# Kernel optimization log

Hardware: AMD Instinct MI355X
Metric: run time of the kernel (lower is better)

Reference implementation:

```python
import jax, jax.numpy as jnp
import numpy as np

EPS = 1e-8  # EPSILON in original repo (sharpen denom); cosine eps matches torch default 1e-8
MAX_SHIFT = 1
M_FEAT = 128


def _lstm_cell(x, h, c, W_ih, W_hh, b_ih, b_hh):
    gates = x @ W_ih.T + b_ih + h @ W_hh.T + b_hh
    i, f, g, o = jnp.split(gates, 4, axis=1)
    c_new = jax.nn.sigmoid(f) * c + jax.nn.sigmoid(i) * jnp.tanh(g)
    h_new = jax.nn.sigmoid(o) * jnp.tanh(c_new)
    return h_new, c_new


def _content_address(bank, k, b):
    # torch cosine_similarity over dim 2: dot / max(|m||k|, eps)
    dot = jnp.einsum('bnm,bm->bn', bank, k)
    denom = jnp.maximum(jnp.linalg.norm(bank, axis=2) * jnp.linalg.norm(k, axis=1, keepdims=True), 1e-8)
    return jax.nn.softmax(b * dot / denom, axis=1)


def _shift(w, s):
    # circular unroll then valid cross-correlation with per-batch kernel s [B, 2*MAX_SHIFT+1]
    wp = jnp.concatenate([w[:, -MAX_SHIFT:], w, w[:, :MAX_SHIFT]], axis=1)
    N = w.shape[1]
    taps = 2 * MAX_SHIFT + 1
    return sum(s[:, i:i + 1] * wp[:, i:i + N] for i in range(taps))


def _sharpen(w, r):
    wr = w ** r
    return wr / (wr.sum(axis=1, keepdims=True) + EPS)


def _move(bank, w_prev, k, b, g, s, r):
    w = _content_address(bank, k, b)
    w = w + (1.0 - g) * w_prev  # faithful: w_c is NOT scaled by g in the source
    w = _shift(w, s)
    return _sharpen(w, r)


def _split_read(p):
    M = M_FEAT
    k = p[:, :M]
    b = jax.nn.softplus(p[:, M:M + 1])
    g = jax.nn.sigmoid(p[:, M + 1:M + 2])
    s = jax.nn.softmax(p[:, M + 2:M + 5], axis=1)
    r = 1.0 + jax.nn.softplus(p[:, M + 5:M + 6])
    return k, b, g, s, r


def _split_write(p):
    M = M_FEAT
    k, b, g, s, r = _split_read(p[:, :M + 6])
    e = jax.nn.sigmoid(p[:, M + 6:M + 6 + M])
    a = p[:, M + 6 + M:M + 6 + 2 * M]
    return k, b, g, s, r, e, a


def setup_inputs() -> dict:
    key = jax.random.key(0)
    ks = jax.random.split(key, 16)
    B, E, H, N, M, O = 64, 256, 512, 4096, 128, 256
    rd_out, wr_out = M + 2 * MAX_SHIFT + 4, 3 * M + 2 * MAX_SHIFT + 4
    sc = 0.05
    return {
        'x': jax.random.normal(ks[0], (B, E), jnp.float32),
        'h_prev': jax.random.normal(ks[1], (B, H), jnp.float32),
        'c_prev': jax.random.normal(ks[2], (B, H), jnp.float32),
        'bank': jax.random.normal(ks[3], (B, N, M), jnp.float32) * 0.1,
        'read_w_prev': jnp.zeros((3, B, N), jnp.float32),
        'write_w_prev': jnp.zeros((3, B, N), jnp.float32),
        'W_ih': jax.random.normal(ks[4], (4 * H, E), jnp.float32) * sc,
        'W_hh': jax.random.normal(ks[5], (4 * H, H), jnp.float32) * sc,
        'b_ih': jax.random.normal(ks[6], (4 * H,), jnp.float32) * sc,
        'b_hh': jax.random.normal(ks[7], (4 * H,), jnp.float32) * sc,
        'read_W': jax.random.normal(ks[8], (3, rd_out, H), jnp.float32) * sc,
        'read_b': jax.random.normal(ks[9], (3, rd_out), jnp.float32) * sc,
        'write_W': jax.random.normal(ks[10], (3, wr_out, H), jnp.float32) * sc,
        'write_b': jax.random.normal(ks[11], (3, wr_out), jnp.float32) * sc,
        'out_W': jax.random.normal(ks[12], (O, 3 * M + H), jnp.float32) * sc,
        'out_b': jax.random.normal(ks[13], (O,), jnp.float32) * sc,
    }


def reference(x, h_prev, c_prev, bank, read_w_prev, write_w_prev,
              W_ih, W_hh, b_ih, b_hh, read_W, read_b, write_W, write_b,
              out_W, out_b):
    h, c = _lstm_cell(x, h_prev, c_prev, W_ih, W_hh, b_ih, b_hh)
    reads = []
    for i in range(3):  # head_num=3, structurally distinct params per head
        # write head: update bank
        pw = h @ write_W[i].T + write_b[i]
        k, b, g, s, r, e, a = _split_write(pw)
        ww = _move(bank, write_w_prev[i], k, b, g, s, r)
        bank = bank * (1.0 - ww[:, :, None] * e[:, None, :]) + ww[:, :, None] * a[:, None, :]
        # read head: read from updated bank
        pr = h @ read_W[i].T + read_b[i]
        k, b, g, s, r = _split_read(pr)
        wr = _move(bank, read_w_prev[i], k, b, g, s, r)
        reads.append(jnp.einsum('bn,bnm->bm', wr, bank))
    out = jnp.concatenate(reads + [h], axis=1) @ out_W.T + out_b
    return out
```

## Files before the change

### kernel.cpp

```cpp
#include <hip/hip_runtime.h>
#include <math.h>

namespace {

constexpr int kB = 64;
constexpr int kN = 4096;
constexpr int kM = 128;
constexpr int kH = 512;
constexpr int kE = 256;
constexpr int kO = 256;
constexpr int kGates = 4 * kH;
constexpr int kCatW = 3 * kM + kH;
constexpr int kPRow = 1600;
constexpr int kWN = kB * kN;

__device__ __forceinline__ float sigm_(float x) { return 1.f / (1.f + expf(-x)); }
__device__ __forceinline__ float softplus_(float x) { return x > 20.f ? x : log1pf(expf(x)); }

__global__ __launch_bounds__(256) void gates_gemm(const float* __restrict__ x,
                                                  const float* __restrict__ W_ih,
                                                  const float* __restrict__ h_prev,
                                                  const float* __restrict__ W_hh,
                                                  float* __restrict__ gates,
                                                  const float* __restrict__ out_b,
                                                  float* __restrict__ out,
                                                  float* __restrict__ cat) {
  if (blockIdx.x == 32) {
    const int tid = threadIdx.x;
    for (int i = tid; i < kB * kO; i += 256) out[i] = out_b[i & (kO - 1)];
    for (int i = tid; i < kB * 384; i += 256) cat[(i / 384) * kCatW + (i % 384)] = 0.f;
    return;
  }
  __shared__ float As[64][68];
  __shared__ float Ws[64][68];
  const int tid = threadIdx.x;
  const int j0 = blockIdx.x * 64;
  const int b0 = (tid & 15) * 4;
  const int j4 = (tid >> 4) * 4;
  float acc[4][4] = {};
  for (int kc = 0; kc < 12; kc++) {
    const bool isx = kc < 4;
    const float* A = isx ? x : h_prev;
    const float* W = isx ? W_ih : W_hh;
    const int lda = isx ? kE : kH;
    const int k0 = (isx ? kc : (kc - 4)) * 64;
    __syncthreads();
#pragma unroll
    for (int i = 0; i < 4; i++) {
      int idx = tid + i * 256;
      int bb = idx >> 4;
      int kk = (idx & 15) * 4;
      float4 v = *(const float4*)(A + (size_t)bb * lda + k0 + kk);
      As[kk][bb] = v.x; As[kk + 1][bb] = v.y; As[kk + 2][bb] = v.z; As[kk + 3][bb] = v.w;
      float4 w = *(const float4*)(W + (size_t)(j0 + bb) * lda + k0 + kk);
      Ws[kk][bb] = w.x; Ws[kk + 1][bb] = w.y; Ws[kk + 2][bb] = w.z; Ws[kk + 3][bb] = w.w;
    }
    __syncthreads();
#pragma unroll 2
    for (int k = 0; k < 64; k++) {
      float4 av = *(const float4*)&As[k][b0];
      float4 wv = *(const float4*)&Ws[k][j4];
      float aa[4] = {av.x, av.y, av.z, av.w};
      float ww[4] = {wv.x, wv.y, wv.z, wv.w};
#pragma unroll
      for (int ii = 0; ii < 4; ii++)
#pragma unroll
        for (int jj = 0; jj < 4; jj++) acc[ii][jj] += aa[ii] * ww[jj];
    }
  }
#pragma unroll
  for (int ii = 0; ii < 4; ii++) {
    float4 st = make_float4(acc[ii][0], acc[ii][1], acc[ii][2], acc[ii][3]);
    *(float4*)&gates[(size_t)(b0 + ii) * kGates + j0 + j4] = st;
  }
}

__global__ __launch_bounds__(256) void lstm_nl(const float* __restrict__ gates,
                                               const float* __restrict__ b_ih,
                                               const float* __restrict__ b_hh,
                                               const float* __restrict__ c_prev,
                                               float* __restrict__ cat) {
  int idx = blockIdx.x * 256 + threadIdx.x;
  if (idx >= kB * kH) return;
  int b = idx >> 9;
  int hh = idx & (kH - 1);
  const float* g = gates + (size_t)b * kGates;
  float i_ = g[hh]          + b_ih[hh]          + b_hh[hh];
  float f_ = g[kH + hh]     + b_ih[kH + hh]     + b_hh[kH + hh];
  float g_ = g[2 * kH + hh] + b_ih[2 * kH + hh] + b_hh[2 * kH + hh];
  float o_ = g[3 * kH + hh] + b_ih[3 * kH + hh] + b_hh[3 * kH + hh];
  float c = sigm_(f_) * c_prev[idx] + sigm_(i_) * tanhf(g_);
  cat[(size_t)b * kCatW + 3 * kM + hh] = sigm_(o_) * tanhf(c);
}

__global__ __launch_bounds__(256) void proj_gemm(const float* __restrict__ cat,
                                                 const float* __restrict__ write_W,
                                                 const float* __restrict__ read_W,
                                                 float* __restrict__ praw) {
  __shared__ float As[64][68];
  __shared__ float Ws[64][68];
  const float* A = cat + 3 * kM;
  const int tid = threadIdx.x;
  const int j0 = blockIdx.x * 64;
  const int b0 = (tid & 15) * 4;
  const int j4 = (tid >> 4) * 4;
  float acc[4][4] = {};
  for (int kc = 0; kc < 8; kc++) {
    const int k0 = kc * 64;
    __syncthreads();
#pragma unroll
    for (int i = 0; i < 4; i++) {
      int idx = tid + i * 256;
      int bb = idx >> 4;
      int kk = (idx & 15) * 4;
      float4 v = *(const float4*)(A + (size_t)bb * kCatW + k0 + kk);
      As[kk][bb] = v.x; As[kk + 1][bb] = v.y; As[kk + 2][bb] = v.z; As[kk + 3][bb] = v.w;
      int j = j0 + bb;
      float4 w = make_float4(0.f, 0.f, 0.f, 0.f);
      if (j < 1170)      w = *(const float4*)(write_W + (size_t)j * kH + k0 + kk);
      else if (j < 1572) w = *(const float4*)(read_W + (size_t)(j - 1170) * kH + k0 + kk);
      Ws[kk][bb] = w.x; Ws[kk + 1][bb] = w.y; Ws[kk + 2][bb] = w.z; Ws[kk + 3][bb] = w.w;
    }
    __syncthreads();
#pragma unroll 2
    for (int k = 0; k < 64; k++) {
      float4 av = *(const float4*)&As[k][b0];
      float4 wv = *(const float4*)&Ws[k][j4];
      float aa[4] = {av.x, av.y, av.z, av.w};
      float ww[4] = {wv.x, wv.y, wv.z, wv.w};
#pragma unroll
      for (int ii = 0; ii < 4; ii++)
#pragma unroll
        for (int jj = 0; jj < 4; jj++) acc[ii][jj] += aa[ii] * ww[jj];
    }
  }
  if (j0 + j4 < 1572) {
#pragma unroll
    for (int ii = 0; ii < 4; ii++) {
      float4 st = make_float4(acc[ii][0], acc[ii][1], acc[ii][2], acc[ii][3]);
      *(float4*)&praw[(size_t)(b0 + ii) * kPRow + j0 + j4] = st;
    }
  }
}

__global__ __launch_bounds__(128) void split_params(const float* __restrict__ praw,
                                                    const float* __restrict__ write_b,
                                                    const float* __restrict__ read_b,
                                                    float* __restrict__ kwb, float* __restrict__ krb,
                                                    float* __restrict__ evb, float* __restrict__ avb,
                                                    float* __restrict__ scal,
                                                    float* __restrict__ sdot) {
  const int b = blockIdx.x;
  const int m = threadIdx.x;
  __shared__ float red[2];
  for (int i = 0; i < 3; i++) {
    const float* p = praw + (size_t)b * kPRow + i * 390;
    const float* wb = write_b + i * 390;
    float kv = p[m] + wb[m];
    kwb[((size_t)i * kB + b) * kM + m] = kv;
    evb[((size_t)i * kB + b) * kM + m] = sigm_(p[134 + m] + wb[134 + m]);
    avb[((size_t)i * kB + b) * kM + m] = p[262 + m] + wb[262 + m];
    float sq = kv * kv;
#pragma unroll
    for (int mm = 1; mm < 64; mm <<= 1) sq += __shfl_xor(sq, mm, 64);
    __syncthreads();
    if ((m & 63) == 0) red[m >> 6] = sq;
    __syncthreads();
    if (m == 0) {
      float* s = scal + ((size_t)i * kB + b) * 8;
      s[0] = softplus_(p[128] + wb[128]);
      s[1] = sigm_(p[129] + wb[129]);
      s[2] = 1.f + softplus_(p[133] + wb[133]);
      float x0 = p[130] + wb[130], x1 = p[131] + wb[131], x2 = p[132] + wb[132];
      float mx = fmaxf(x0, fmaxf(x1, x2));
      float e0 = expf(x0 - mx), e1 = expf(x1 - mx), e2 = expf(x2 - mx);
      float si = 1.f / (e0 + e1 + e2);
      s[3] = e0 * si; s[4] = e1 * si; s[5] = e2 * si;
      s[6] = sqrtf(red[0] + red[1]);
    }
    __syncthreads();
  }
  for (int i = 0; i < 3; i++) {
    const float* p = praw + (size_t)b * kPRow + 1170 + i * 134;
    const float* rb = read_b + i * 134;
    float kv = p[m] + rb[m];
    krb[((size_t)i * kB + b) * kM + m] = kv;
    float sq = kv * kv;
#pragma unroll
    for (int mm = 1; mm < 64; mm <<= 1) sq += __shfl_xor(sq, mm, 64);
    __syncthreads();
    if ((m & 63) == 0) red[m >> 6] = sq;
    __syncthreads();
    if (m == 0) {
      float* s = scal + ((size_t)(3 + i) * kB + b) * 8;
      s[0] = softplus_(p[128] + rb[128]);
      s[1] = sigm_(p[129] + rb[129]);
      s[2] = 1.f + softplus_(p[133] + rb[133]);
      float x0 = p[130] + rb[130], x1 = p[131] + rb[131], x2 = p[132] + rb[132];
      float mx = fmaxf(x0, fmaxf(x1, x2));
      float e0 = expf(x0 - mx), e1 = expf(x1 - mx), e2 = expf(x2 - mx);
      float si = 1.f / (e0 + e1 + e2);
      s[3] = e0 * si; s[4] = e1 * si; s[5] = e2 * si;
      s[6] = sqrtf(red[0] + red[1]);
    }
    __syncthreads();
  }
  __syncthreads();
  if (m < 64) {
    const float* a0 = avb + ((size_t)0 * kB + b) * kM;
    const float* a2 = avb + ((size_t)2 * kB + b) * kM;
    const float* u[5] = {a0, a0, a0, a2, a2};
    const float* v[5] = {krb + ((size_t)0 * kB + b) * kM,
                         kwb + ((size_t)1 * kB + b) * kM,
                         a0,
                         krb + ((size_t)2 * kB + b) * kM,
                         a2};
#pragma unroll
    for (int d = 0; d < 5; d++) {
      float s = u[d][m] * v[d][m] + u[d][m + 64] * v[d][m + 64];
#pragma unroll
      for (int mm = 1; mm < 64; mm <<= 1) s += __shfl_xor(s, mm, 64);
      if (m == 0) sdot[b * 8 + d] = s;
    }
  }
}

__global__ __launch_bounds__(256) void passA_k(const float* __restrict__ bank,
                                               const float* __restrict__ kwb,
                                               const float* __restrict__ krb,
                                               const float* __restrict__ evb,
                                               const float* __restrict__ avb,
                                               float* __restrict__ mA) {
  const int b = blockIdx.y, chunk = blockIdx.x;
  const int tid = threadIdx.x;
  const int lane = tid & 63, wv = tid >> 6, sub = lane >> 4, lm = lane & 15;
  const int m8 = lm * 8;
  float kw0r[8], kr0r[8], kw1r[8], a0r[8], e0r[8];
#pragma unroll
  for (int t = 0; t < 8; t++) {
    kw0r[t] = kwb[((size_t)0 * kB + b) * kM + m8 + t];
    kr0r[t] = krb[((size_t)0 * kB + b) * kM + m8 + t];
    kw1r[t] = kwb[((size_t)1 * kB + b) * kM + m8 + t];
    a0r[t]  = avb[((size_t)0 * kB + b) * kM + m8 + t];
    e0r[t]  = evb[((size_t)0 * kB + b) * kM + m8 + t];
  }
  const size_t bbase = (size_t)b * kN * kM;
  const size_t brow = (size_t)b * kN;
  for (int it = 0; it < 16; it++) {
    const int row = chunk * 256 + it * 16 + wv * 4 + sub;
    const float* rp = bank + bbase + (size_t)row * kM + m8;
    float4 u0 = *(const float4*)rp;
    float4 u1 = *(const float4*)(rp + 4);
    float v[8] = {u0.x, u0.y, u0.z, u0.w, u1.x, u1.y, u1.z, u1.w};
    float s[10] = {};
#pragma unroll
    for (int t = 0; t < 8; t++) {
      float be = v[t] * e0r[t];
      s[0] += v[t] * kw0r[t];
      s[1] += v[t] * v[t];
      s[2] += v[t] * kr0r[t];
      s[3] += be * kr0r[t];
      s[4] += v[t] * kw1r[t];
      s[5] += be * kw1r[t];
      s[6] += be * v[t];
      s[7] += be * be;
      s[8] += v[t] * a0r[t];
      s[9] += be * a0r[t];
    }
#pragma unroll
    for (int m = 1; m < 16; m <<= 1)
#pragma unroll
      for (int k = 0; k < 10; k++) s[k] += __shfl_xor(s[k], m, 64);
    if (lm == 0) {
#pragma unroll
      for (int k = 0; k < 10; k++) mA[(size_t)k * kWN + brow + row] = s[k];
    }
  }
}

__device__ void addr_core(int tid, float* loc, const float* sc, const float* __restrict__ wp,
                          float* wb, float* red) {
  const float g = sc[1], r = sc[2];
  const float s0 = sc[3], s1 = sc[4], s2 = sc[5];
  const int lane = tid & 63, wid = tid >> 6;
  __syncthreads();
  float mx = -1e30f;
#pragma unroll
  for (int i = 0; i < 16; i++) mx = fmaxf(mx, loc[i]);
#pragma unroll
  for (int m = 1; m < 64; m <<= 1) mx = fmaxf(mx, __shfl_xor(mx, m, 64));
  if (lane == 0) red[wid] = mx;
  __syncthreads();
  mx = fmaxf(fmaxf(red[0], red[1]), fmaxf(red[2], red[3]));
  float sum = 0.f;
#pragma unroll
  for (int i = 0; i < 16; i++) { loc[i] = expf(loc[i] - mx); sum += loc[i]; }
#pragma unroll
  for (int m = 1; m < 64; m <<= 1) sum += __shfl_xor(sum, m, 64);
  __syncthreads();
  if (lane == 0) red[wid] = sum;
  __syncthreads();
  sum = red[0] + red[1] + red[2] + red[3];
  const float inv = 1.f / sum;
  const float omg = 1.f - g;
#pragma unroll
  for (int i = 0; i < 16; i++) {
    int n = tid + i * 256;
    wb[n] = loc[i] * inv + omg * wp[n];
  }
  __syncthreads();
  float ssum = 0.f;
#pragma unroll
  for (int i = 0; i < 16; i++) {
    int n = tid + i * 256;
    float sh = s0 * wb[(n + kN - 1) & (kN - 1)] + s1 * wb[n] + s2 * wb[(n + 1) & (kN - 1)];
    float y = powf(sh, r);
    loc[i] = y;
    ssum += y;
  }
#pragma unroll
  for (int m = 1; m < 64; m <<= 1) ssum += __shfl_xor(ssum, m, 64);
  __syncthreads();
  if (lane == 0) red[wid] = ssum;
  __syncthreads();
  ssum = red[0] + red[1] + red[2] + red[3];
  const float invs = 1.f / (ssum + 1e-8f);
#pragma unroll
  for (int i = 0; i < 16; i++) loc[i] *= invs;
}

__global__ __launch_bounds__(256) void a12_k(const float* __restrict__ mA,
                                             const float* __restrict__ scal,
                                             const float* __restrict__ sdot,
                                             const float* __restrict__ read_w_prev,
                                             const float* __restrict__ write_w_prev,
                                             float* __restrict__ wwv,
                                             float* __restrict__ wrv) {
  const int b = blockIdx.x;
  const int tid = threadIdx.x;
  __shared__ float wb[kN];
  __shared__ float red[4];
  const size_t brow = (size_t)b * kN;
  float loc[16], w0r[16], q1r[16];
  {
    const float* sc = scal + ((size_t)0 * kB + b) * 8;
    const float beta = sc[0], kn = sc[6];
#pragma unroll
    for (int i = 0; i < 16; i++) {
      size_t idx = brow + tid + i * 256;
      float d = mA[0 * (size_t)kWN + idx];
      float q = mA[1 * (size_t)kWN + idx];
      loc[i] = beta * d / fmaxf(sqrtf(fmaxf(q, 0.f)) * kn, 1e-8f);
    }
    addr_core(tid, loc, sc, write_w_prev + brow, wb, red);
#pragma unroll
    for (int i = 0; i < 16; i++) { wwv[brow + tid + i * 256] = loc[i]; w0r[i] = loc[i]; }
  }
  {
    const float* sc = scal + ((size_t)3 * kB + b) * 8;
    const float beta = sc[0], kn = sc[6];
    const float sa0kr0 = sdot[b * 8 + 0], sa0a0 = sdot[b * 8 + 2];
#pragma unroll
    for (int i = 0; i < 16; i++) {
      size_t idx = brow + tid + i * 256;
      float w0 = w0r[i], w0q = w0 * w0;
      float q1 = mA[1 * (size_t)kWN + idx]
               - 2.f * w0 * mA[6 * (size_t)kWN + idx]
               + w0q * mA[7 * (size_t)kWN + idx]
               + 2.f * w0 * mA[8 * (size_t)kWN + idx]
               - 2.f * w0q * mA[9 * (size_t)kWN + idx]
               + w0q * sa0a0;
      q1r[i] = q1;
      float d = mA[2 * (size_t)kWN + idx] - w0 * mA[3 * (size_t)kWN + idx] + w0 * sa0kr0;
      loc[i] = beta * d / fmaxf(sqrtf(fmaxf(q1, 0.f)) * kn, 1e-8f);
    }
    addr_core(tid, loc, sc, read_w_prev + brow, wb, red);
#pragma unroll
    for (int i = 0; i < 16; i++) wrv[brow + tid + i * 256] = loc[i];
  }
  {
    const float* sc = scal + ((size_t)1 * kB + b) * 8;
    const float beta = sc[0], kn = sc[6];
    const float sa0kw1 = sdot[b * 8 + 1];
#pragma unroll
    for (int i = 0; i < 16; i++) {
      size_t idx = brow + tid + i * 256;
      float w0 = w0r[i];
      float d = mA[4 * (size_t)kWN + idx] - w0 * mA[5 * (size_t)kWN + idx] + w0 * sa0kw1;
      loc[i] = beta * d / fmaxf(sqrtf(fmaxf(q1r[i], 0.f)) * kn, 1e-8f);
    }
    addr_core(tid, loc, sc, write_w_prev + kWN + brow, wb, red);
#pragma unroll
    for (int i = 0; i < 16; i++) wwv[kWN + brow + tid + i * 256] = loc[i];
  }
}

__global__ __launch_bounds__(256) void passB_k(const float* __restrict__ bank,
                                               const float* __restrict__ wwv,
                                               const float* __restrict__ wrv,
                                               const float* __restrict__ kwb,
                                               const float* __restrict__ krb,
                                               const float* __restrict__ evb,
                                               const float* __restrict__ avb,
                                               float* __restrict__ cat,
                                               float* __restrict__ mB) {
  const int b = blockIdx.y, chunk = blockIdx.x;
  const int tid = threadIdx.x;
  const int lane = tid & 63, wv = tid >> 6, sub = lane >> 4, lm = lane & 15;
  const int m8 = lm * 8;
  float e0r[8], a0r[8], e1r[8], a1r[8], kr1r[8], kw2r[8], kr2r[8], e2r[8], a2r[8];
#pragma unroll
  for (int t = 0; t < 8; t++) {
    e0r[t]  = evb[((size_t)0 * kB + b) * kM + m8 + t];
    a0r[t]  = avb[((size_t)0 * kB + b) * kM + m8 + t];
    e1r[t]  = evb[((size_t)1 * kB + b) * kM + m8 + t];
    a1r[t]  = avb[((size_t)1 * kB + b) * kM + m8 + t];
    kr1r[t] = krb[((size_t)1 * kB + b) * kM + m8 + t];
    kw2r[t] = kwb[((size_t)2 * kB + b) * kM + m8 + t];
    kr2r[t] = krb[((size_t)2 * kB + b) * kM + m8 + t];
    e2r[t]  = evb[((size_t)2 * kB + b) * kM + m8 + t];
    a2r[t]  = avb[((size_t)2 * kB + b) * kM + m8 + t];
  }
  float racc[8] = {};
  __shared__ float rlds[kM];
  if (tid < kM) rlds[tid] = 0.f;
  const size_t bbase = (size_t)b * kN * kM;
  const size_t brow = (size_t)b * kN;
  for (int it = 0; it < 16; it++) {
    const int row = chunk * 256 + it * 16 + wv * 4 + sub;
    const float* rp = bank + bbase + (size_t)row * kM + m8;
    float4 u0 = *(const float4*)rp;
    float4 u1 = *(const float4*)(rp + 4);
    float v[8] = {u0.x, u0.y, u0.z, u0.w, u1.x, u1.y, u1.z, u1.w};
    const float w0 = wwv[brow + row];
    const float w1 = wwv[kWN + brow + row];
    const float wr0 = wrv[brow + row];
#pragma unroll
    for (int t = 0; t < 8; t++) {
      v[t] += w0 * (a0r[t] - e0r[t] * v[t]);
      racc[t] += wr0 * v[t];
      v[t] += w1 * (a1r[t] - e1r[t] * v[t]);
    }
    float s[9] = {};
#pragma unroll
    for (int t = 0; t < 8; t++) {
      float ve = v[t] * e2r[t];
      s[0] += v[t] * kr1r[t];
      s[1] += v[t] * kw2r[t];
      s[2] += v[t] * v[t];
      s[3] += v[t] * kr2r[t];
      s[4] += ve * kr2r[t];
      s[5] += ve * v[t];
      s[6] += ve * ve;
      s[7] += v[t] * a2r[t];
      s[8] += ve * a2r[t];
    }
#pragma unroll
    for (int m = 1; m < 16; m <<= 1)
#pragma unroll
      for (int k = 0; k < 9; k++) s[k] += __shfl_xor(s[k], m, 64);
    if (lm == 0) {
#pragma unroll
      for (int k = 0; k < 9; k++) mB[(size_t)k * kWN + brow + row] = s[k];
    }
  }
  __syncthreads();
#pragma unroll
  for (int t = 0; t < 8; t++) {
    racc[t] += __shfl_xor(racc[t], 16, 64);
    racc[t] += __shfl_xor(racc[t], 32, 64);
  }
  if (sub == 0) {
#pragma unroll
    for (int t = 0; t < 8; t++) atomicAdd(&rlds[m8 + t], racc[t]);
  }
  __syncthreads();
  if (tid < kM) atomicAdd(&cat[(size_t)b * kCatW + tid], rlds[tid]);
}

__global__ __launch_bounds__(256) void a34_k(const float* __restrict__ mB,
                                             const float* __restrict__ scal,
                                             const float* __restrict__ sdot,
                                             const float* __restrict__ read_w_prev,
                                             const float* __restrict__ write_w_prev,
                                             float* __restrict__ wwv,
                                             float* __restrict__ wrv) {
  const int b = blockIdx.x;
  const int tid = threadIdx.x;
  __shared__ float wb[kN];
  __shared__ float red[4];
  const size_t brow = (size_t)b * kN;
  float loc[16], w2r[16];
  {
    const float* sc = scal + ((size_t)4 * kB + b) * 8;
    const float beta = sc[0], kn = sc[6];
#pragma unroll
    for (int i = 0; i < 16; i++) {
      size_t idx = brow + tid + i * 256;
      float d = mB[0 * (size_t)kWN + idx];
      float q = mB[2 * (size_t)kWN + idx];
      loc[i] = beta * d / fmaxf(sqrtf(fmaxf(q, 0.f)) * kn, 1e-8f);
    }
    addr_core(tid, loc, sc, read_w_prev + kWN + brow, wb, red);
#pragma unroll
    for (int i = 0; i < 16; i++) wrv[kWN + brow + tid + i * 256] = loc[i];
  }
  {
    const float* sc = scal + ((size_t)2 * kB + b) * 8;
    const float beta = sc[0], kn = sc[6];
#pragma unroll
    for (int i = 0; i < 16; i++) {
      size_t idx = brow + tid + i * 256;
      float d = mB[1 * (size_t)kWN + idx];
      float q = mB[2 * (size_t)kWN + idx];
      loc[i] = beta * d / fmaxf(sqrtf(fmaxf(q, 0.f)) * kn, 1e-8f);
    }
    addr_core(tid, loc, sc, write_w_prev + 2 * kWN + brow, wb, red);
#pragma unroll
    for (int i = 0; i < 16; i++) { wwv[2 * (size_t)kWN + brow + tid + i * 256] = loc[i]; w2r[i] = loc[i]; }
  }
  {
    const float* sc = scal + ((size_t)5 * kB + b) * 8;
    const float beta = sc[0], kn = sc[6];
    const float sa2kr2 = sdot[b * 8 + 3], sa2a2 = sdot[b * 8 + 4];
#pragma unroll
    for (int i = 0; i < 16; i++) {
      size_t idx = brow + tid + i * 256;
      float w2 = w2r[i], w2q = w2 * w2;
      float q3 = mB[2 * (size_t)kWN + idx]
               - 2.f * w2 * mB[5 * (size_t)kWN + idx]
               + w2q * mB[6 * (size_t)kWN + idx]
               + 2.f * w2 * mB[7 * (size_t)kWN + idx]
               - 2.f * w2q * mB[8 * (size_t)kWN + idx]
               + w2q * sa2a2;
      float d = mB[3 * (size_t)kWN + idx] - w2 * mB[4 * (size_t)kWN + idx] + w2 * sa2kr2;
      loc[i] = beta * d / fmaxf(sqrtf(fmaxf(q3, 0.f)) * kn, 1e-8f);
    }
    addr_core(tid, loc, sc, read_w_prev + 2 * kWN + brow, wb, red);
#pragma unroll
    for (int i = 0; i < 16; i++) wrv[2 * (size_t)kWN + brow + tid + i * 256] = loc[i];
  }
}

__global__ __launch_bounds__(256) void passC_k(const float* __restrict__ bank,
                                               const float* __restrict__ wwv,
                                               const float* __restrict__ wrv,
                                               const float* __restrict__ evb,
                                               const float* __restrict__ avb,
                                               float* __restrict__ cat) {
  const int b = blockIdx.y, chunk = blockIdx.x;
  const int tid = threadIdx.x;
  const int lane = tid & 63, wv = tid >> 6, sub = lane >> 4, lm = lane & 15;
  const int m8 = lm * 8;
  float e_r[3][8], a_r[3][8];
#pragma unroll
  for (int j = 0; j < 3; j++)
#pragma unroll
    for (int t = 0; t < 8; t++) {
      e_r[j][t] = evb[((size_t)j * kB + b) * kM + m8 + t];
      a_r[j][t] = avb[((size_t)j * kB + b) * kM + m8 + t];
    }
  float racc1[8] = {}, racc2[8] = {};
  __shared__ float rlds[2][kM];
  if (tid < kM) { rlds[0][tid] = 0.f; rlds[1][tid] = 0.f; }
  const size_t bbase = (size_t)b * kN * kM;
  const size_t brow = (size_t)b * kN;
  for (int it = 0; it < 16; it++) {
    const int row = chunk * 256 + it * 16 + wv * 4 + sub;
    const float* rp = bank + bbase + (size_t)row * kM + m8;
    float4 u0 = *(const float4*)rp;
    float4 u1 = *(const float4*)(rp + 4);
    float v[8] = {u0.x, u0.y, u0.z, u0.w, u1.x, u1.y, u1.z, u1.w};
    const float w0 = wwv[brow + row];
    const float w1 = wwv[kWN + brow + row];
    const float w2 = wwv[2 * (size_t)kWN + brow + row];
    const float wr1 = wrv[kWN + brow + row];
    const float wr2 = wrv[2 * (size_t)kWN + brow + row];
#pragma unroll
    for (int t = 0; t < 8; t++) {
      v[t] += w0 * (a_r[0][t] - e_r[0][t] * v[t]);
      v[t] += w1 * (a_r[1][t] - e_r[1][t] * v[t]);
      racc1[t] += wr1 * v[t];
      v[t] += w2 * (a_r[2][t] - e_r[2][t] * v[t]);
      racc2[t] += wr2 * v[t];
    }
  }
  __syncthreads();
#pragma unroll
  for (int t = 0; t < 8; t++) {
    racc1[t] += __shfl_xor(racc1[t], 16, 64);
    racc1[t] += __shfl_xor(racc1[t], 32, 64);
    racc2[t] += __shfl_xor(racc2[t], 16, 64);
    racc2[t] += __shfl_xor(racc2[t], 32, 64);
  }
  if (sub == 0) {
#pragma unroll
    for (int t = 0; t < 8; t++) {
      atomicAdd(&rlds[0][m8 + t], racc1[t]);
      atomicAdd(&rlds[1][m8 + t], racc2[t]);
    }
  }
  __syncthreads();
  if (tid < kM) {
    atomicAdd(&cat[(size_t)b * kCatW + kM + tid], rlds[0][tid]);
    atomicAdd(&cat[(size_t)b * kCatW + 2 * kM + tid], rlds[1][tid]);
  }
}

__global__ __launch_bounds__(256) void out_gemm(const float* __restrict__ A,
                                                const float* __restrict__ W,
                                                float* __restrict__ C) {
  __shared__ float As[64][68];
  __shared__ float Ws[64][68];
  const int tid = threadIdx.x;
  const int j0 = blockIdx.x * 64;
  const int b0 = (tid & 15) * 4;
  const int j4 = (tid >> 4) * 4;
  float acc[4][4] = {};
  for (int kc = 0; kc < 2; kc++) {
    const int k0 = blockIdx.y * 128 + kc * 64;
    __syncthreads();
#pragma unroll
    for (int i = 0; i < 4; i++) {
      int idx = tid + i * 256;
      int bb = idx >> 4;
      int kk = (idx & 15) * 4;
      float4 v = *(const float4*)(A + (size_t)bb * kCatW + k0 + kk);
      As[kk][bb] = v.x; As[kk + 1][bb] = v.y; As[kk + 2][bb] = v.z; As[kk + 3][bb] = v.w;
      float4 w = *(const float4*)(W + (size_t)(j0 + bb) * kCatW + k0 + kk);
      Ws[kk][bb] = w.x; Ws[kk + 1][bb] = w.y; Ws[kk + 2][bb] = w.z; Ws[kk + 3][bb] = w.w;
    }
    __syncthreads();
#pragma unroll 2
    for (int k = 0; k < 64; k++) {
      float4 av = *(const float4*)&As[k][b0];
      float4 wv = *(const float4*)&Ws[k][j4];
      float aa[4] = {av.x, av.y, av.z, av.w};
      float ww[4] = {wv.x, wv.y, wv.z, wv.w};
#pragma unroll
      for (int ii = 0; ii < 4; ii++)
#pragma unroll
        for (int jj = 0; jj < 4; jj++) acc[ii][jj] += aa[ii] * ww[jj];
    }
  }
#pragma unroll
  for (int ii = 0; ii < 4; ii++)
#pragma unroll
    for (int jj = 0; jj < 4; jj++)
      atomicAdd(&C[(size_t)(b0 + ii) * kO + j0 + j4 + jj], acc[ii][jj]);
}

}

extern "C" void kernel_launch(void* const* d_in, const int* in_sizes, int n_in,
                              void* d_out, int out_size, void* d_ws, size_t ws_size,
                              hipStream_t stream) {
  const float* x            = (const float*)d_in[0];
  const float* h_prev       = (const float*)d_in[1];
  const float* c_prev       = (const float*)d_in[2];
  const float* bank         = (const float*)d_in[3];
  const float* read_w_prev  = (const float*)d_in[4];
  const float* write_w_prev = (const float*)d_in[5];
  const float* W_ih         = (const float*)d_in[6];
  const float* W_hh         = (const float*)d_in[7];
  const float* b_ih         = (const float*)d_in[8];
  const float* b_hh         = (const float*)d_in[9];
  const float* read_W       = (const float*)d_in[10];
  const float* read_b       = (const float*)d_in[11];
  const float* write_W      = (const float*)d_in[12];
  const float* write_b      = (const float*)d_in[13];
  const float* out_W        = (const float*)d_in[14];
  const float* out_b        = (const float*)d_in[15];
  float* out = (float*)d_out;

  float* ws    = (float*)d_ws;
  float* gates = ws;
  float* praw  = gates + kB * kGates;
  float* cat   = praw + kB * kPRow;
  float* kwb   = cat + kB * kCatW;
  float* krb   = kwb + 3 * kB * kM;
  float* evb   = krb + 3 * kB * kM;
  float* avb   = evb + 3 * kB * kM;
  float* scal  = avb + 3 * kB * kM;
  float* sdot  = scal + 6 * kB * 8;
  float* wwv   = sdot + kB * 8;
  float* wrv   = wwv + 3 * kWN;
  float* mA    = wrv + 3 * kWN;
  float* mB    = mA + 10 * (size_t)kWN;

  gates_gemm<<<33, 256, 0, stream>>>(x, W_ih, h_prev, W_hh, gates, out_b, out, cat);
  lstm_nl<<<(kB * kH) / 256, 256, 0, stream>>>(gates, b_ih, b_hh, c_prev, cat);
  proj_gemm<<<25, 256, 0, stream>>>(cat, write_W, read_W, praw);
  split_params<<<64, 128, 0, stream>>>(praw, write_b, read_b, kwb, krb, evb, avb, scal, sdot);

  passA_k<<<dim3(16, kB), 256, 0, stream>>>(bank, kwb, krb, evb, avb, mA);
  a12_k<<<64, 256, 0, stream>>>(mA, scal, sdot, read_w_prev, write_w_prev, wwv, wrv);
  passB_k<<<dim3(16, kB), 256, 0, stream>>>(bank, wwv, wrv, kwb, krb, evb, avb, cat, mB);
  a34_k<<<64, 256, 0, stream>>>(mB, scal, sdot, read_w_prev, write_w_prev, wwv, wrv);
  passC_k<<<dim3(16, kB), 256, 0, stream>>>(bank, wwv, wrv, evb, avb, cat);
  out_gemm<<<dim3(kO / 64, kCatW / 128), 256, 0, stream>>>(cat, out_W, out);

  (void)in_sizes; (void)n_in; (void)out_size; (void)ws_size;
}
```

Measured before the change: 490.4 us.

## Prefetch bank rows in passes and widen addressing kernels to 1024 threads

The three bank-streaming passes now software-prefetch the next row's float4 data and weights into registers while the current row is being computed, and carry a launch_bounds occupancy hint. The addressing kernels a12/a34 move from 256 to 1024 threads per block, so each thread handles 4 elements instead of 16 and the reductions run across 16 waves. The softmax uses exp2f and pow is replaced by exp2(r*log2), with zero inputs mapped to zero. The prefetch adds register pressure, and the serial 64-block addressing kernels gain parallelism at the cost of wider block reductions.

```diff
diff --git a/kernel.cpp b/kernel.cpp
--- a/kernel.cpp
+++ b/kernel.cpp
@@ -13,6 +13,7 @@
 constexpr int kCatW = 3 * kM + kH;
 constexpr int kPRow = 1600;
 constexpr int kWN = kB * kN;
+constexpr float kLog2e = 1.4426950408889634f;
 
 __device__ __forceinline__ float sigm_(float x) { return 1.f / (1.f + expf(-x)); }
 __device__ __forceinline__ float softplus_(float x) { return x > 20.f ? x : log1pf(expf(x)); }
@@ -225,12 +226,12 @@
   }
 }
 
-__global__ __launch_bounds__(256) void passA_k(const float* __restrict__ bank,
-                                               const float* __restrict__ kwb,
-                                               const float* __restrict__ krb,
-                                               const float* __restrict__ evb,
-                                               const float* __restrict__ avb,
-                                               float* __restrict__ mA) {
+__global__ __launch_bounds__(256, 4) void passA_k(const float* __restrict__ bank,
+                                                  const float* __restrict__ kwb,
+                                                  const float* __restrict__ krb,
+                                                  const float* __restrict__ evb,
+                                                  const float* __restrict__ avb,
+                                                  float* __restrict__ mA) {
   const int b = blockIdx.y, chunk = blockIdx.x;
   const int tid = threadIdx.x;
   const int lane = tid & 63, wv = tid >> 6, sub = lane >> 4, lm = lane & 15;
@@ -246,12 +247,18 @@
   }
   const size_t bbase = (size_t)b * kN * kM;
   const size_t brow = (size_t)b * kN;
+  const int row0 = chunk * 256 + wv * 4 + sub;
+  const float* rp = bank + bbase + (size_t)row0 * kM + m8;
+  float4 c0 = *(const float4*)rp;
+  float4 c1 = *(const float4*)(rp + 4);
   for (int it = 0; it < 16; it++) {
-    const int row = chunk * 256 + it * 16 + wv * 4 + sub;
-    const float* rp = bank + bbase + (size_t)row * kM + m8;
-    float4 u0 = *(const float4*)rp;
-    float4 u1 = *(const float4*)(rp + 4);
-    float v[8] = {u0.x, u0.y, u0.z, u0.w, u1.x, u1.y, u1.z, u1.w};
+    float v[8] = {c0.x, c0.y, c0.z, c0.w, c1.x, c1.y, c1.z, c1.w};
+    if (it < 15) {
+      const float* np = bank + bbase + (size_t)(row0 + (it + 1) * 16) * kM + m8;
+      c0 = *(const float4*)np;
+      c1 = *(const float4*)(np + 4);
+    }
+    const int row = row0 + it * 16;
     float s[10] = {};
 #pragma unroll
     for (int t = 0; t < 8; t++) {
@@ -278,43 +285,45 @@
   }
 }
 
-__device__ void addr_core(int tid, float* loc, const float* sc, const float* __restrict__ wp,
-                          float* wb, float* red) {
+__device__ void addr_core4(int tid, float* loc, const float* sc, const float* __restrict__ wp,
+                           float* wb, float* red) {
   const float g = sc[1], r = sc[2];
-  const float s0 = sc[3], s1 = sc[4], s2 = sc[5];
+  const float s0 = sc[3], s1c = sc[4], s2 = sc[5];
   const int lane = tid & 63, wid = tid >> 6;
   __syncthreads();
-  float mx = -1e30f;
-#pragma unroll
-  for (int i = 0; i < 16; i++) mx = fmaxf(mx, loc[i]);
+  float mx = fmaxf(fmaxf(loc[0], loc[1]), fmaxf(loc[2], loc[3]));
 #pragma unroll
   for (int m = 1; m < 64; m <<= 1) mx = fmaxf(mx, __shfl_xor(mx, m, 64));
   if (lane == 0) red[wid] = mx;
   __syncthreads();
-  mx = fmaxf(fmaxf(red[0], red[1]), fmaxf(red[2], red[3]));
+  mx = red[0];
+#pragma unroll
+  for (int k = 1; k < 16; k++) mx = fmaxf(mx, red[k]);
   float sum = 0.f;
 #pragma unroll
-  for (int i = 0; i < 16; i++) { loc[i] = expf(loc[i] - mx); sum += loc[i]; }
+  for (int i = 0; i < 4; i++) { loc[i] = exp2f((loc[i] - mx) * kLog2e); sum += loc[i]; }
 #pragma unroll
   for (int m = 1; m < 64; m <<= 1) sum += __shfl_xor(sum, m, 64);
   __syncthreads();
   if (lane == 0) red[wid] = sum;
   __syncthreads();
-  sum = red[0] + red[1] + red[2] + red[3];
+  sum = red[0];
+#pragma unroll
+  for (int k = 1; k < 16; k++) sum += red[k];
   const float inv = 1.f / sum;
   const float omg = 1.f - g;
 #pragma unroll
-  for (int i = 0; i < 16; i++) {
-    int n = tid + i * 256;
+  for (int i = 0; i < 4; i++) {
+    int n = tid + i * 1024;
     wb[n] = loc[i] * inv + omg * wp[n];
   }
   __syncthreads();
   float ssum = 0.f;
 #pragma unroll
-  for (int i = 0; i < 16; i++) {
-    int n = tid + i * 256;
-    float sh = s0 * wb[(n + kN - 1) & (kN - 1)] + s1 * wb[n] + s2 * wb[(n + 1) & (kN - 1)];
-    float y = powf(sh, r);
+  for (int i = 0; i < 4; i++) {
+    int n = tid + i * 1024;
+    float sh = s0 * wb[(n + kN - 1) & (kN - 1)] + s1c * wb[n] + s2 * wb[(n + 1) & (kN - 1)];
+    float y = (sh > 0.f) ? exp2f(r * log2f(sh)) : 0.f;
     loc[i] = y;
     ssum += y;
   }
@@ -323,46 +332,49 @@
   __syncthreads();
   if (lane == 0) red[wid] = ssum;
   __syncthreads();
-  ssum = red[0] + red[1] + red[2] + red[3];
+  ssum = red[0];
+#pragma unroll
+  for (int k = 1; k < 16; k++) ssum += red[k];
   const float invs = 1.f / (ssum + 1e-8f);
 #pragma unroll
-  for (int i = 0; i < 16; i++) loc[i] *= invs;
-}
-
-__global__ __launch_bounds__(256) void a12_k(const float* __restrict__ mA,
-                                             const float* __restrict__ scal,
-                                             const float* __restrict__ sdot,
-                                             const float* __restrict__ read_w_prev,
-                                             const float* __restrict__ write_w_prev,
-                                             float* __restrict__ wwv,
-                                             float* __restrict__ wrv) {
+  for (int i = 0; i < 4; i++) loc[i] *= invs;
+  __syncthreads();
+}
+
+__global__ __launch_bounds__(1024) void a12_k(const float* __restrict__ mA,
+                                              const float* __restrict__ scal,
+                                              const float* __restrict__ sdot,
+                                              const float* __restrict__ read_w_prev,
+                                              const float* __restrict__ write_w_prev,
+                                              float* __restrict__ wwv,
+                                              float* __restrict__ wrv) {
   const int b = blockIdx.x;
   const int tid = threadIdx.x;
   __shared__ float wb[kN];
-  __shared__ float red[4];
+  __shared__ float red[16];
   const size_t brow = (size_t)b * kN;
-  float loc[16], w0r[16], q1r[16];
+  float loc[4], w0r[4], q1r[4];
   {
     const float* sc = scal + ((size_t)0 * kB + b) * 8;
     const float beta = sc[0], kn = sc[6];
 #pragma unroll
-    for (int i = 0; i < 16; i++) {
-      size_t idx = brow + tid + i * 256;
+    for (int i = 0; i < 4; i++) {
+      size_t idx = brow + tid + i * 1024;
       float d = mA[0 * (size_t)kWN + idx];
       float q = mA[1 * (size_t)kWN + idx];
       loc[i] = beta * d / fmaxf(sqrtf(fmaxf(q, 0.f)) * kn, 1e-8f);
     }
-    addr_core(tid, loc, sc, write_w_prev + brow, wb, red);
-#pragma unroll
-    for (int i = 0; i < 16; i++) { wwv[brow + tid + i * 256] = loc[i]; w0r[i] = loc[i]; }
+    addr_core4(tid, loc, sc, write_w_prev + brow, wb, red);
+#pragma unroll
+    for (int i = 0; i < 4; i++) { wwv[brow + tid + i * 1024] = loc[i]; w0r[i] = loc[i]; }
   }
   {
     const float* sc = scal + ((size_t)3 * kB + b) * 8;
     const float beta = sc[0], kn = sc[6];
     const float sa0kr0 = sdot[b * 8 + 0], sa0a0 = sdot[b * 8 + 2];
 #pragma unroll
-    for (int i = 0; i < 16; i++) {
-      size_t idx = brow + tid + i * 256;
+    for (int i = 0; i < 4; i++) {
+      size_t idx = brow + tid + i * 1024;
       float w0 = w0r[i], w0q = w0 * w0;
       float q1 = mA[1 * (size_t)kWN + idx]
                - 2.f * w0 * mA[6 * (size_t)kWN + idx]
@@ -374,36 +386,36 @@
       float d = mA[2 * (size_t)kWN + idx] - w0 * mA[3 * (size_t)kWN + idx] + w0 * sa0kr0;
       loc[i] = beta * d / fmaxf(sqrtf(fmaxf(q1, 0.f)) * kn, 1e-8f);
     }
-    addr_core(tid, loc, sc, read_w_prev + brow, wb, red);
-#pragma unroll
-    for (int i = 0; i < 16; i++) wrv[brow + tid + i * 256] = loc[i];
+    addr_core4(tid, loc, sc, read_w_prev + brow, wb, red);
+#pragma unroll
+    for (int i = 0; i < 4; i++) wrv[brow + tid + i * 1024] = loc[i];
   }
   {
     const float* sc = scal + ((size_t)1 * kB + b) * 8;
     const float beta = sc[0], kn = sc[6];
     const float sa0kw1 = sdot[b * 8 + 1];
 #pragma unroll
-    for (int i = 0; i < 16; i++) {
-      size_t idx = brow + tid + i * 256;
+    for (int i = 0; i < 4; i++) {
+      size_t idx = brow + tid + i * 1024;
       float w0 = w0r[i];
       float d = mA[4 * (size_t)kWN + idx] - w0 * mA[5 * (size_t)kWN + idx] + w0 * sa0kw1;
       loc[i] = beta * d / fmaxf(sqrtf(fmaxf(q1r[i], 0.f)) * kn, 1e-8f);
     }
-    addr_core(tid, loc, sc, write_w_prev + kWN + brow, wb, red);
-#pragma unroll
-    for (int i = 0; i < 16; i++) wwv[kWN + brow + tid + i * 256] = loc[i];
-  }
-}
-
-__global__ __launch_bounds__(256) void passB_k(const float* __restrict__ bank,
-                                               const float* __restrict__ wwv,
-                                               const float* __restrict__ wrv,
-                                               const float* __restrict__ kwb,
-                                               const float* __restrict__ krb,
-                                               const float* __restrict__ evb,
-                                               const float* __restrict__ avb,
-                                               float* __restrict__ cat,
-                                               float* __restrict__ mB) {
+    addr_core4(tid, loc, sc, write_w_prev + kWN + brow, wb, red);
+#pragma unroll
+    for (int i = 0; i < 4; i++) wwv[kWN + brow + tid + i * 1024] = loc[i];
+  }
+}
+
+__global__ __launch_bounds__(256, 4) void passB_k(const float* __restrict__ bank,
+                                                  const float* __restrict__ wwv,
+                                                  const float* __restrict__ wrv,
+                                                  const float* __restrict__ kwb,
+                                                  const float* __restrict__ krb,
+                                                  const float* __restrict__ evb,
+                                                  const float* __restrict__ avb,
+                                                  float* __restrict__ cat,
+                                                  float* __restrict__ mB) {
   const int b = blockIdx.y, chunk = blockIdx.x;
   const int tid = threadIdx.x;
   const int lane = tid & 63, wv = tid >> 6, sub = lane >> 4, lm = lane & 15;
@@ -426,15 +438,26 @@
   if (tid < kM) rlds[tid] = 0.f;
   const size_t bbase = (size_t)b * kN * kM;
   const size_t brow = (size_t)b * kN;
+  const int row0 = chunk * 256 + wv * 4 + sub;
+  const float* rp = bank + bbase + (size_t)row0 * kM + m8;
+  float4 c0 = *(const float4*)rp;
+  float4 c1 = *(const float4*)(rp + 4);
+  float w0p = wwv[brow + row0];
+  float w1p = wwv[kWN + brow + row0];
+  float wr0p = wrv[brow + row0];
   for (int it = 0; it < 16; it++) {
-    const int row = chunk * 256 + it * 16 + wv * 4 + sub;
-    const float* rp = bank + bbase + (size_t)row * kM + m8;
-    float4 u0 = *(const float4*)rp;
-    float4 u1 = *(const float4*)(rp + 4);
-    float v[8] = {u0.x, u0.y, u0.z, u0.w, u1.x, u1.y, u1.z, u1.w};
-    const float w0 = wwv[brow + row];
-    const float w1 = wwv[kWN + brow + row];
-    const float wr0 = wrv[brow + row];
+    float v[8] = {c0.x, c0.y, c0.z, c0.w, c1.x, c1.y, c1.z, c1.w};
+    const float w0 = w0p, w1 = w1p, wr0 = wr0p;
+    if (it < 15) {
+      const int nrow = row0 + (it + 1) * 16;
+      const float* np = bank + bbase + (size_t)nrow * kM + m8;
+      c0 = *(const float4*)np;
+      c1 = *(const float4*)(np + 4);
+      w0p = wwv[brow + nrow];
+      w1p = wwv[kWN + brow + nrow];
+      wr0p = wrv[brow + nrow];
+    }
+    const int row = row0 + it * 16;
 #pragma unroll
     for (int t = 0; t < 8; t++) {
       v[t] += w0 * (a0r[t] - e0r[t] * v[t]);
@@ -478,54 +501,54 @@
   if (tid < kM) atomicAdd(&cat[(size_t)b * kCatW + tid], rlds[tid]);
 }
 
-__global__ __launch_bounds__(256) void a34_k(const float* __restrict__ mB,
-                                             const float* __restrict__ scal,
-                                             const float* __restrict__ sdot,
-                                             const float* __restrict__ read_w_prev,
-                                             const float* __restrict__ write_w_prev,
-                                             float* __restrict__ wwv,
-                                             float* __restrict__ wrv) {
+__global__ __launch_bounds__(1024) void a34_k(const float* __restrict__ mB,
+                                              const float* __restrict__ scal,
+                                              const float* __restrict__ sdot,
+                                              const float* __restrict__ read_w_prev,
+                                              const float* __restrict__ write_w_prev,
+                                              float* __restrict__ wwv,
+                                              float* __restrict__ wrv) {
   const int b = blockIdx.x;
   const int tid = threadIdx.x;
   __shared__ float wb[kN];
-  __shared__ float red[4];
+  __shared__ float red[16];
   const size_t brow = (size_t)b * kN;
-  float loc[16], w2r[16];
+  float loc[4], w2r[4];
   {
     const float* sc = scal + ((size_t)4 * kB + b) * 8;
     const float beta = sc[0], kn = sc[6];
 #pragma unroll
-    for (int i = 0; i < 16; i++) {
-      size_t idx = brow + tid + i * 256;
+    for (int i = 0; i < 4; i++) {
+      size_t idx = brow + tid + i * 1024;
       float d = mB[0 * (size_t)kWN + idx];
       float q = mB[2 * (size_t)kWN + idx];
       loc[i] = beta * d / fmaxf(sqrtf(fmaxf(q, 0.f)) * kn, 1e-8f);
     }
-    addr_core(tid, loc, sc, read_w_prev + kWN + brow, wb, red);
-#pragma unroll
-    for (int i = 0; i < 16; i++) wrv[kWN + brow + tid + i * 256] = loc[i];
+    addr_core4(tid, loc, sc, read_w_prev + kWN + brow, wb, red);
+#pragma unroll
+    for (int i = 0; i < 4; i++) wrv[kWN + brow + tid + i * 1024] = loc[i];
   }
   {
     const float* sc = scal + ((size_t)2 * kB + b) * 8;
     const float beta = sc[0], kn = sc[6];
 #pragma unroll
-    for (int i = 0; i < 16; i++) {
-      size_t idx = brow + tid + i * 256;
+    for (int i = 0; i < 4; i++) {
+      size_t idx = brow + tid + i * 1024;
       float d = mB[1 * (size_t)kWN + idx];
       float q = mB[2 * (size_t)kWN + idx];
       loc[i] = beta * d / fmaxf(sqrtf(fmaxf(q, 0.f)) * kn, 1e-8f);
     }
-    addr_core(tid, loc, sc, write_w_prev + 2 * kWN + brow, wb, red);
-#pragma unroll
-    for (int i = 0; i < 16; i++) { wwv[2 * (size_t)kWN + brow + tid + i * 256] = loc[i]; w2r[i] = loc[i]; }
+    addr_core4(tid, loc, sc, write_w_prev + 2 * kWN + brow, wb, red);
+#pragma unroll
+    for (int i = 0; i < 4; i++) { wwv[2 * (size_t)kWN + brow + tid + i * 1024] = loc[i]; w2r[i] = loc[i]; }
   }
   {
     const float* sc = scal + ((size_t)5 * kB + b) * 8;
     const float beta = sc[0], kn = sc[6];
     const float sa2kr2 = sdot[b * 8 + 3], sa2a2 = sdot[b * 8 + 4];
 #pragma unroll
-    for (int i = 0; i < 16; i++) {
-      size_t idx = brow + tid + i * 256;
+    for (int i = 0; i < 4; i++) {
+      size_t idx = brow + tid + i * 1024;
       float w2 = w2r[i], w2q = w2 * w2;
       float q3 = mB[2 * (size_t)kWN + idx]
                - 2.f * w2 * mB[5 * (size_t)kWN + idx]
@@ -536,18 +559,18 @@
       float d = mB[3 * (size_t)kWN + idx] - w2 * mB[4 * (size_t)kWN + idx] + w2 * sa2kr2;
       loc[i] = beta * d / fmaxf(sqrtf(fmaxf(q3, 0.f)) * kn, 1e-8f);
     }
-    addr_core(tid, loc, sc, read_w_prev + 2 * kWN + brow, wb, red);
-#pragma unroll
-    for (int i = 0; i < 16; i++) wrv[2 * (size_t)kWN + brow + tid + i * 256] = loc[i];
-  }
-}
-
-__global__ __launch_bounds__(256) void passC_k(const float* __restrict__ bank,
-                                               const float* __restrict__ wwv,
-                                               const float* __restrict__ wrv,
-                                               const float* __restrict__ evb,
-                                               const float* __restrict__ avb,
-                                               float* __restrict__ cat) {
+    addr_core4(tid, loc, sc, read_w_prev + 2 * kWN + brow, wb, red);
+#pragma unroll
+    for (int i = 0; i < 4; i++) wrv[2 * (size_t)kWN + brow + tid + i * 1024] = loc[i];
+  }
+}
+
+__global__ __launch_bounds__(256, 4) void passC_k(const float* __restrict__ bank,
+                                                  const float* __restrict__ wwv,
+                                                  const float* __restrict__ wrv,
+                                                  const float* __restrict__ evb,
+                                                  const float* __restrict__ avb,
+                                                  float* __restrict__ cat) {
   const int b = blockIdx.y, chunk = blockIdx.x;
   const int tid = threadIdx.x;
   const int lane = tid & 63, wv = tid >> 6, sub = lane >> 4, lm = lane & 15;
@@ -565,17 +588,29 @@
   if (tid < kM) { rlds[0][tid] = 0.f; rlds[1][tid] = 0.f; }
   const size_t bbase = (size_t)b * kN * kM;
   const size_t brow = (size_t)b * kN;
+  const int row0 = chunk * 256 + wv * 4 + sub;
+  const float* rp = bank + bbase + (size_t)row0 * kM + m8;
+  float4 c0 = *(const float4*)rp;
+  float4 c1 = *(const float4*)(rp + 4);
+  float w0p = wwv[brow + row0];
+  float w1p = wwv[kWN + brow + row0];
+  float w2p = wwv[2 * (size_t)kWN + brow + row0];
+  float wr1p = wrv[kWN + brow + row0];
+  float wr2p = wrv[2 * (size_t)kWN + brow + row0];
   for (int it = 0; it < 16; it++) {
-    const int row = chunk * 256 + it * 16 + wv * 4 + sub;
-    const float* rp = bank + bbase + (size_t)row * kM + m8;
-    float4 u0 = *(const float4*)rp;
-    float4 u1 = *(const float4*)(rp + 4);
-    float v[8] = {u0.x, u0.y, u0.z, u0.w, u1.x, u1.y, u1.z, u1.w};
-    const float w0 = wwv[brow + row];
-    const float w1 = wwv[kWN + brow + row];
-    const float w2 = wwv[2 * (size_t)kWN + brow + row];
-    const float wr1 = wrv[kWN + brow + row];
-    const float wr2 = wrv[2 * (size_t)kWN + brow + row];
+    float v[8] = {c0.x, c0.y, c0.z, c0.w, c1.x, c1.y, c1.z, c1.w};
+    const float w0 = w0p, w1 = w1p, w2 = w2p, wr1 = wr1p, wr2 = wr2p;
+    if (it < 15) {
+      const int nrow = row0 + (it + 1) * 16;
+      const float* np = bank + bbase + (size_t)nrow * kM + m8;
+      c0 = *(const float4*)np;
+      c1 = *(const float4*)(np + 4);
+      w0p = wwv[brow + nrow];
+      w1p = wwv[kWN + brow + nrow];
+      w2p = wwv[2 * (size_t)kWN + brow + nrow];
+      wr1p = wrv[kWN + brow + nrow];
+      wr2p = wrv[2 * (size_t)kWN + brow + nrow];
+    }
 #pragma unroll
     for (int t = 0; t < 8; t++) {
       v[t] += w0 * (a_r[0][t] - e_r[0][t] * v[t]);
@@ -694,9 +729,9 @@
   split_params<<<64, 128, 0, stream>>>(praw, write_b, read_b, kwb, krb, evb, avb, scal, sdot);
 
   passA_k<<<dim3(16, kB), 256, 0, stream>>>(bank, kwb, krb, evb, avb, mA);
-  a12_k<<<64, 256, 0, stream>>>(mA, scal, sdot, read_w_prev, write_w_prev, wwv, wrv);
+  a12_k<<<64, 1024, 0, stream>>>(mA, scal, sdot, read_w_prev, write_w_prev, wwv, wrv);
   passB_k<<<dim3(16, kB), 256, 0, stream>>>(bank, wwv, wrv, kwb, krb, evb, avb, cat, mB);
-  a34_k<<<64, 256, 0, stream>>>(mB, scal, sdot, read_w_prev, write_w_prev, wwv, wrv);
+  a34_k<<<64, 1024, 0, stream>>>(mB, scal, sdot, read_w_prev, write_w_prev, wwv, wrv);
   passC_k<<<dim3(16, kB), 256, 0, stream>>>(bank, wwv, wrv, evb, avb, cat);
   out_gemm<<<dim3(kO / 64, kCatW / 128), 256, 0, stream>>>(cat, out_W, out);
 
```

Result: faster. 445.2 us (-9.2%).
